# Kernel optimization log

Hardware: AMD Instinct MI355X
Metric: run time of the kernel (lower is better)

Reference implementation:

```python
import jax, jax.numpy as jnp
import numpy as np

NUM_GROUPS = 4   # temporal frames == deformable groups
K = 3            # deformable / fusion kernel size
PAD = 1
MAX_DISP = 7
STRIDE2 = 2


def _conv2d(x, w):
    # 3x3, stride 1, pad 1, no bias, NCHW/OIHW
    return jax.lax.conv_general_dilated(
        x, w, window_strides=(1, 1), padding=((PAD, PAD), (PAD, PAD)),
        dimension_numbers=("NCHW", "OIHW", "NCHW"))


def _correlation(x1, x2):
    """FlowNet/PWC correlation: kernel_size=1, max_displacement=7, stride1=1, stride2=2.
    Output: [B, 49, H, W], mean over channels of shifted dot products."""
    B, C, H, W = x1.shape
    r = MAX_DISP // STRIDE2          # 3 -> 7x7 displacement grid
    m = r * STRIDE2                  # 6 = max shift magnitude
    x2p = jnp.pad(x2, ((0, 0), (0, 0), (m, m), (m, m)))
    outs = []
    for di in range(-r, r + 1):
        for dj in range(-r, r + 1):
            dy, dx = di * STRIDE2, dj * STRIDE2
            sh = x2p[:, :, m + dy:m + dy + H, m + dx:m + dx + W]
            outs.append(jnp.mean(x1 * sh, axis=1))
    return jnp.stack(outs, axis=1)   # [B, 49, H, W]


def _deform_conv(x, offset, weight):
    """Deformable conv v1 (ConvOffset2d): 3x3, stride 1, pad 1, NUM_GROUPS deformable groups.
    offset: [B, G*2*K*K, H, W] laid out as (g, k, {dy,dx})."""
    B, C, H, W = x.shape
    G, K2 = NUM_GROUPS, K * K
    Cg = C // G
    off = offset.reshape(B, G, K2, 2, H, W)
    rel = (jnp.arange(K) - PAD).astype(x.dtype)
    rel_y = jnp.repeat(rel, K).reshape(1, 1, K2, 1, 1)   # kh-major, matches weight flatten
    rel_x = jnp.tile(rel, K).reshape(1, 1, K2, 1, 1)
    iy = jnp.arange(H, dtype=x.dtype).reshape(1, 1, 1, H, 1)
    ix = jnp.arange(W, dtype=x.dtype).reshape(1, 1, 1, 1, W)
    py = iy + rel_y + off[:, :, :, 0]   # [B,G,K2,H,W] sample rows
    px = ix + rel_x + off[:, :, :, 1]   # sample cols
    xg = x.reshape(B, G, Cg, H, W).transpose(0, 1, 3, 4, 2)  # [B,G,H,W,Cg]
    y0 = jnp.floor(py); x0 = jnp.floor(px)
    fy = py - y0; fx = px - x0
    y0 = y0.astype(jnp.int32); x0 = x0.astype(jnp.int32)
    bi = jnp.arange(B).reshape(B, 1, 1, 1, 1)
    gi = jnp.arange(G).reshape(1, G, 1, 1, 1)
    acc = jnp.zeros((B, G, K2, H, W, Cg), x.dtype)
    for dy in (0, 1):
        for dx in (0, 1):
            yy = y0 + dy; xx = x0 + dx
            wgt = (fy if dy else 1.0 - fy) * (fx if dx else 1.0 - fx)
            valid = ((yy >= 0) & (yy < H) & (xx >= 0) & (xx < W)).astype(x.dtype)
            v = xg[bi, gi, jnp.clip(yy, 0, H - 1), jnp.clip(xx, 0, W - 1)]
            acc = acc + v * (wgt * valid)[..., None]
    wr = weight.reshape(weight.shape[0], G, Cg, K2)  # [O,G,Cg,K2]
    return jnp.einsum('bgkhwc,ogck->bohw', acc, wr)


def setup_inputs() -> dict:
    key = jax.random.key(0)
    k0, k1, k2, k3 = jax.random.split(key, 4)
    B, C, H, W = 4, 256, 64, 64
    G = NUM_GROUPS
    inputs = jax.random.normal(k0, (B * G, C, H, W), jnp.float32)
    w_offset = jax.random.normal(k1, (G * 2 * K * K, C + MAX_DISP ** 2, K, K), jnp.float32) * 0.02
    w_def = jax.random.normal(k2, (C, C, K, K), jnp.float32) * 0.02
    w_fusion = jax.random.normal(k3, (C, C * G, K, K), jnp.float32) * 0.02
    return {"inputs": inputs, "w_offset": w_offset, "w_def": w_def,
            "w_fusion": w_fusion, "d1": 0, "d2": 0}


def reference(inputs, w_offset, w_def, w_fusion, d1, d2):
    # d1, d2 are unused by the original forward.
    G = NUM_GROUPS
    y = inputs[G - 1::G]
    _y = jax.lax.stop_gradient(y)
    feats = []
    for ii in range(G - 1):           # n_iter = 1
        x = inputs[ii::G]
        _x = jax.lax.stop_gradient(x)
        corr = _correlation(_x, _y)                       # [B,49,H,W]
        off = _conv2d(jnp.concatenate([x, corr], axis=1), w_offset)
        x = _deform_conv(x, off, w_def)
        feats.append(x)
    return _conv2d(jnp.concatenate(feats + [y], axis=1), w_fusion)
```

## Files before the change

kernel.cpp:

```cpp
#include <hip/hip_runtime.h>

#define HH 64
#define WW 64
#define HW 4096
#define CC 256
#define BB 4
#define GG 4
#define NPAIR 3

typedef __attribute__((ext_vector_type(8))) short short8;
typedef __attribute__((ext_vector_type(4))) float f32x4;
typedef unsigned short ushort_t;

__device__ inline ushort_t f2bf(float x) {
    unsigned int u = __float_as_uint(x);
    unsigned int r = (u + 0x7fffu + ((u >> 16) & 1u)) >> 16;
    return (ushort_t)r;
}
__device__ inline float bflo(unsigned u) { return __uint_as_float(u << 16); }
__device__ inline float bfhi(unsigned u) { return __uint_as_float(u & 0xffff0000u); }

__global__ void prep_wdef(const float* __restrict__ wd, ushort_t* __restrict__ wmf) {
    int idx = blockIdx.x * 256 + threadIdx.x;
    if (idx >= 9 * 256 * 256) return;
    int k = idx >> 16;
    int rem = idx & 65535;
    int o = rem >> 8;
    int c = rem & 255;
    wmf[idx] = f2bf(wd[((size_t)(o * 256 + c)) * 9 + k]);
}

__global__ void prep_woff(const float* __restrict__ wo, ushort_t* __restrict__ wmf) {
    int idx = blockIdx.x * 256 + threadIdx.x;
    if (idx >= 9 * 80 * 320) return;
    int k = idx / (80 * 320);
    int rem = idx % (80 * 320);
    int o = rem / 320;
    int ci = rem % 320;
    wmf[idx] = (o < 72 && ci < 305) ? f2bf(wo[((size_t)o * 305 + ci) * 9 + k]) : (ushort_t)0;
}

__global__ void prep_wfus(const float* __restrict__ wf, ushort_t* __restrict__ wmf) {
    int idx = blockIdx.x * 256 + threadIdx.x;
    if (idx >= 9 * 256 * 1024) return;
    int k = idx / (256 * 1024);
    int rem = idx % (256 * 1024);
    int o = rem / 1024;
    int ci = rem % 1024;
    wmf[idx] = f2bf(wf[((size_t)o * 1024 + ci) * 9 + k]);
}

__global__ void __launch_bounds__(256) xt_build(const float* __restrict__ in,
                                                ushort_t* __restrict__ XT) {
    __shared__ ushort_t tileT[64][72];
    int hw0 = blockIdx.x * 64;
    int ct = blockIdx.y;
    int z = blockIdx.z;
    int pair = z >> 2, b = z & 3;
    int t = threadIdx.x;
    int cil = t >> 2, q = t & 3;
    const float* sp = in + ((size_t)(b * 4 + pair) * 256 + ct * 64 + cil) * HW + hw0 + q * 16;
#pragma unroll
    for (int i = 0; i < 16; ++i) tileT[q * 16 + i][cil] = f2bf(sp[i]);
    __syncthreads();
    int hwl = t >> 2;
    const uint4* tp = reinterpret_cast<const uint4*>(&tileT[hwl][q * 16]);
    uint4* op = reinterpret_cast<uint4*>(
        &XT[((size_t)z * HW + hw0 + hwl) * 320 + ct * 64 + q * 16]);
    op[0] = tp[0];
    op[1] = tp[1];
}

__global__ void __launch_bounds__(256, 8) corr_partial(const float* __restrict__ in,
                                                       float* __restrict__ P) {
    __shared__ float x1l[8][64];
    __shared__ float x2l[8][7][76];
    int h = blockIdx.x, z = blockIdx.y, cg = blockIdx.z;
    int pair = z >> 2, b = z & 3;
    const float* x1 = in + (size_t)(b * GG + pair) * CC * HW + h * WW;
    const float* x2 = in + (size_t)(b * GG + 3) * CC * HW;
    int tid = threadIdx.x;
    int w = tid & 63;
    int dg = tid >> 6;

    float acc[2][7];
#pragma unroll
    for (int i = 0; i < 2; ++i)
#pragma unroll
        for (int j = 0; j < 7; ++j) acc[i][j] = 0.f;

    for (int c0 = cg * 64; c0 < cg * 64 + 64; c0 += 8) {
        __syncthreads();
#pragma unroll
        for (int idx = tid; idx < 512; idx += 256) {
            int cc = idx >> 6, ww = idx & 63;
            x1l[cc][ww] = x1[(size_t)(c0 + cc) * HW + ww];
        }
        for (int idx = tid; idx < 8 * 7 * 76; idx += 256) {
            int cc = idx / 532;
            int rem = idx - cc * 532;
            int r = rem / 76;
            int cl = rem - r * 76;
            int row = h + 2 * (r - 3);
            int col = cl - 6;
            float v = 0.f;
            if (row >= 0 && row < HH && col >= 0 && col < WW)
                v = x2[(size_t)(c0 + cc) * HW + row * WW + col];
            x2l[cc][r][cl] = v;
        }
        __syncthreads();
#pragma unroll
        for (int cc = 0; cc < 8; ++cc) {
            float x1v = x1l[cc][w];
#pragma unroll
            for (int i = 0; i < 2; ++i) {
                int di = dg * 2 + i;
                if (di < 7) {
#pragma unroll
                    for (int dj = 0; dj < 7; ++dj)
                        acc[i][dj] += x1v * x2l[cc][di][w + 2 * dj];
                }
            }
        }
    }
    float* pp = P + ((size_t)(cg * 12 + z) * 49) * HW + h * WW + w;
#pragma unroll
    for (int i = 0; i < 2; ++i) {
        int di = dg * 2 + i;
        if (di < 7) {
#pragma unroll
            for (int dj = 0; dj < 7; ++dj)
                pp[(size_t)(di * 7 + dj) * HW] = acc[i][dj];
        }
    }
}

__global__ void __launch_bounds__(256) corr_reduce(const float* __restrict__ P,
                                                   ushort_t* __restrict__ XT) {
    int h = blockIdx.x, z = blockIdx.y;
    int tid = threadIdx.x;
    int w = tid & 63;
    int dg = tid >> 6;
    const size_t cgs = (size_t)12 * 49 * HW;
    ushort_t* xrow = XT + ((size_t)z * HW + h * WW + w) * 320;
#pragma unroll
    for (int i = 0; i < 2; ++i) {
        int di = dg * 2 + i;
        if (di < 7) {
#pragma unroll
            for (int dj = 0; dj < 7; ++dj) {
                int d = di * 7 + dj;
                const float* pp = P + ((size_t)z * 49 + d) * HW + h * WW + w;
                float s = pp[0] + pp[cgs] + pp[2 * cgs] + pp[3 * cgs];
                xrow[256 + d] = f2bf(s * (1.f / 256.f));
            }
        }
    }
    if (dg == 3) {
#pragma unroll
        for (int p = 0; p < 15; ++p) xrow[305 + p] = 0;
    }
}

__global__ void __launch_bounds__(256, 2) offconv_mfma(const ushort_t* __restrict__ XT,
                                                       const ushort_t* __restrict__ wmf,
                                                       float* __restrict__ off) {
    __shared__ ushort_t a_lds[9][80][40];
    __shared__ ushort_t b_hal[264][40];
    int lin = (blockIdx.x & 7) * 48 + (blockIdx.x >> 3);
    int z = lin >> 5;
    int n0t = lin & 31;
    int h0 = n0t * 2;
    int t = threadIdx.x;
    int wid = t >> 6;
    int lane = t & 63;
    int l15 = lane & 15;
    int kq = lane >> 4;
    const ushort_t* xtb = XT + (size_t)z * HW * 320;

    f32x4 acc[5][2];
#pragma unroll
    for (int m = 0; m < 5; ++m)
#pragma unroll
        for (int n = 0; n < 2; ++n) acc[m][n] = (f32x4){0.f, 0.f, 0.f, 0.f};

#pragma unroll 1
    for (int cs = 0; cs < 10; ++cs) {
        int ci0 = cs * 32;
        __syncthreads();
        for (int idx = t; idx < 264; idx += 256) {
            int r = idx / 66, c = idx - r * 66;
            int hP = h0 + r - 1, wP = c - 1;
            uint4* dst = reinterpret_cast<uint4*>(&b_hal[idx][0]);
            if (hP >= 0 && hP < HH && wP >= 0 && wP < WW) {
                const uint4* src = reinterpret_cast<const uint4*>(
                    xtb + (size_t)(hP * WW + wP) * 320 + ci0);
                dst[0] = src[0];
                dst[1] = src[1];
                dst[2] = src[2];
                dst[3] = src[3];
            } else {
                uint4 zz = make_uint4(0, 0, 0, 0);
                dst[0] = zz;
                dst[1] = zz;
                dst[2] = zz;
                dst[3] = zz;
            }
        }
        for (int idx = t; idx < 2880; idx += 256) {
            int tp = idx / 320;
            int rem = idx - tp * 320;
            int o = rem >> 2, q = rem & 3;
            *reinterpret_cast<uint4*>(&a_lds[tp][o][q * 8]) =
                *reinterpret_cast<const uint4*>(
                    wmf + ((size_t)tp * 80 + o) * 320 + ci0 + q * 8);
        }
        __syncthreads();
#pragma unroll 1
        for (int tap = 0; tap < 9; ++tap) {
            int kh = tap / 3, kw = tap - kh * 3;
            short8 af[5], bf[2];
#pragma unroll
            for (int m = 0; m < 5; ++m)
                af[m] = *reinterpret_cast<const short8*>(&a_lds[tap][m * 16 + l15][kq * 8]);
#pragma unroll
            for (int n = 0; n < 2; ++n) {
                int p = wid * 32 + n * 16 + l15;
                int pos = ((p >> 6) + kh) * 66 + (p & 63) + kw;
                bf[n] = *reinterpret_cast<const short8*>(&b_hal[pos][kq * 8]);
            }
#pragma unroll
            for (int m = 0; m < 5; ++m)
#pragma unroll
                for (int n = 0; n < 2; ++n)
                    acc[m][n] = __builtin_amdgcn_mfma_f32_16x16x32_bf16(af[m], bf[n],
                                                                        acc[m][n], 0, 0, 0);
        }
    }
    float* ob = off + (size_t)z * 72 * HW + h0 * 64 + wid * 32;
#pragma unroll
    for (int m = 0; m < 5; ++m)
#pragma unroll
        for (int n = 0; n < 2; ++n)
#pragma unroll
            for (int e = 0; e < 4; ++e) {
                int o_l = m * 16 + kq * 4 + e;
                if (o_l < 72) ob[(size_t)o_l * HW + n * 16 + l15] = acc[m][n][e];
            }
}

__global__ void __launch_bounds__(256, 3) deform_mfma(const ushort_t* __restrict__ XT,
                                                      const float* __restrict__ off,
                                                      const ushort_t* __restrict__ wmf,
                                                      ushort_t* __restrict__ FT) {
    __shared__ ushort_t b_lds[64][264];
    int u = blockIdx.x & 7, v = blockIdx.x >> 3;
    int lin = u * 96 + v;
    int z = lin >> 6, h = lin & 63;
    int b = z & 3, pair = z >> 2;

    const ushort_t* xtz = XT + (size_t)z * HW * 320;
    const float* offp = off + (size_t)z * 72 * HW;
    int tid = threadIdx.x;
    int lane = tid & 63;
    int g = tid >> 6;
    int l15 = tid & 15;
    int kq = (tid >> 4) & 3;

    f32x4 acc[4][4];
#pragma unroll
    for (int m = 0; m < 4; ++m)
#pragma unroll
        for (int n = 0; n < 4; ++n) acc[m][n] = (f32x4){0.f, 0.f, 0.f, 0.f};

    for (int k = 0; k < 9; ++k) {
        __syncthreads();
        {
            float oy = offp[(size_t)(g * 18 + k * 2 + 0) * HW + h * WW + lane];
            float ox = offp[(size_t)(g * 18 + k * 2 + 1) * HW + h * WW + lane];
            float py = (float)h + (float)(k / 3 - 1) + oy;
            float px = (float)lane + (float)(k % 3 - 1) + ox;
            float y0f = floorf(py), x0f = floorf(px);
            float fy = py - y0f, fx = px - x0f;
            int y0 = (int)y0f, x0 = (int)x0f;
            int y1 = y0 + 1, x1 = x0 + 1;
            bool vy0 = (y0 >= 0) && (y0 < HH);
            bool vy1 = (y1 >= 0) && (y1 < HH);
            bool vx0 = (x0 >= 0) && (x0 < WW);
            bool vx1 = (x1 >= 0) && (x1 < WW);
            float w00 = (1.f - fy) * (1.f - fx) * ((vy0 && vx0) ? 1.f : 0.f);
            float w01 = (1.f - fy) * fx * ((vy0 && vx1) ? 1.f : 0.f);
            float w10 = fy * (1.f - fx) * ((vy1 && vx0) ? 1.f : 0.f);
            float w11 = fy * fx * ((vy1 && vx1) ? 1.f : 0.f);
            int cy0 = min(max(y0, 0), HH - 1), cy1 = min(max(y1, 0), HH - 1);
            int cx0 = min(max(x0, 0), WW - 1), cx1 = min(max(x1, 0), WW - 1);
            const ushort_t* p00 = xtz + (size_t)(cy0 * WW + cx0) * 320 + g * 64;
            const ushort_t* p01 = xtz + (size_t)(cy0 * WW + cx1) * 320 + g * 64;
            const ushort_t* p10 = xtz + (size_t)(cy1 * WW + cx0) * 320 + g * 64;
            const ushort_t* p11 = xtz + (size_t)(cy1 * WW + cx1) * 320 + g * 64;
#pragma unroll
            for (int c0 = 0; c0 < 64; c0 += 8) {
                uint4 a00 = *reinterpret_cast<const uint4*>(p00 + c0);
                uint4 a01 = *reinterpret_cast<const uint4*>(p01 + c0);
                uint4 a10 = *reinterpret_cast<const uint4*>(p10 + c0);
                uint4 a11 = *reinterpret_cast<const uint4*>(p11 + c0);
                unsigned pw[4];
                const unsigned* u00 = &a00.x;
                const unsigned* u01 = &a01.x;
                const unsigned* u10 = &a10.x;
                const unsigned* u11 = &a11.x;
#pragma unroll
                for (int q = 0; q < 4; ++q) {
                    float s0 = w00 * bflo(u00[q]) + w01 * bflo(u01[q]) +
                               w10 * bflo(u10[q]) + w11 * bflo(u11[q]);
                    float s1 = w00 * bfhi(u00[q]) + w01 * bfhi(u01[q]) +
                               w10 * bfhi(u10[q]) + w11 * bfhi(u11[q]);
                    pw[q] = (unsigned)f2bf(s0) | ((unsigned)f2bf(s1) << 16);
                }
                *reinterpret_cast<uint4*>(&b_lds[lane][g * 64 + c0]) =
                    make_uint4(pw[0], pw[1], pw[2], pw[3]);
            }
        }
        __syncthreads();
        const ushort_t* wkbase = wmf + (size_t)k * 65536 + (size_t)(g * 64) * 256;
#pragma unroll 1
        for (int cs = 0; cs < 8; ++cs) {
            int c0 = cs * 32;
            short8 bfr[4], afr[4];
#pragma unroll
            for (int n = 0; n < 4; ++n)
                bfr[n] = *reinterpret_cast<const short8*>(&b_lds[n * 16 + l15][c0 + kq * 8]);
#pragma unroll
            for (int m = 0; m < 4; ++m)
                afr[m] = *reinterpret_cast<const short8*>(
                    wkbase + (size_t)(m * 16 + l15) * 256 + c0 + kq * 8);
#pragma unroll
            for (int m = 0; m < 4; ++m)
#pragma unroll
                for (int n = 0; n < 4; ++n)
                    acc[m][n] = __builtin_amdgcn_mfma_f32_16x16x32_bf16(afr[m], bfr[n],
                                                                        acc[m][n], 0, 0, 0);
        }
    }
    __syncthreads();
#pragma unroll
    for (int m = 0; m < 4; ++m)
#pragma unroll
        for (int n = 0; n < 4; ++n) {
            unsigned lo = (unsigned)f2bf(acc[m][n][0]) | ((unsigned)f2bf(acc[m][n][1]) << 16);
            unsigned hi = (unsigned)f2bf(acc[m][n][2]) | ((unsigned)f2bf(acc[m][n][3]) << 16);
            uint2 vv = make_uint2(lo, hi);
            *reinterpret_cast<uint2*>(&b_lds[n * 16 + l15][g * 64 + m * 16 + kq * 4]) = vv;
        }
    __syncthreads();
    int wout = tid >> 2, ch = tid & 3;
    ushort_t* dst = FT + ((size_t)b * HW + h * 64 + wout) * 1024 + pair * 256 + ch * 64;
    const ushort_t* srcl = &b_lds[wout][ch * 64];
#pragma unroll
    for (int i = 0; i < 8; ++i) {
        uint4 vv = *reinterpret_cast<const uint4*>(srcl + i * 8);
        *reinterpret_cast<uint4*>(dst + i * 8) = vv;
    }
}

__global__ void __launch_bounds__(256) ft_build_y(const float* __restrict__ in,
                                                  ushort_t* __restrict__ FT) {
    __shared__ ushort_t tileT[64][72];
    int hw0 = blockIdx.x * 64;
    int ct = blockIdx.y;
    int b = blockIdx.z;
    int t = threadIdx.x;
    int cil = t >> 2, q = t & 3;
    const float* sp = in + ((size_t)(b * 4 + 3) * 256 + ct * 64 + cil) * HW + hw0 + q * 16;
#pragma unroll
    for (int i = 0; i < 16; ++i) tileT[q * 16 + i][cil] = f2bf(sp[i]);
    __syncthreads();
    int hwl = t >> 2;
    const uint4* tp = reinterpret_cast<const uint4*>(&tileT[hwl][q * 16]);
    uint4* op = reinterpret_cast<uint4*>(
        &FT[((size_t)b * HW + hw0 + hwl) * 1024 + 768 + ct * 64 + q * 16]);
    op[0] = tp[0];
    op[1] = tp[1];
}

__global__ void __launch_bounds__(256, 2) fusion_mfma(const ushort_t* __restrict__ FT,
                                                      const ushort_t* __restrict__ wmf,
                                                      float* __restrict__ out) {
    __shared__ ushort_t a_lds[9][64][40];
    __shared__ ushort_t b_hal[264][40];
    int lin = ((blockIdx.x & 7) << 6) | (blockIdx.x >> 3);
    int ot = lin & 3;
    int g2 = lin >> 2;
    int n0t = g2 & 31;
    int b = g2 >> 5;
    int o0 = ot * 64;
    int h0 = n0t * 2;
    int t = threadIdx.x;
    int wid = t >> 6;
    int lane = t & 63;
    int l15 = lane & 15;
    int kq = lane >> 4;
    const ushort_t* ftb = FT + (size_t)b * HW * 1024;

    f32x4 acc[4][2];
#pragma unroll
    for (int fm = 0; fm < 4; ++fm)
#pragma unroll
        for (int fn = 0; fn < 2; ++fn) acc[fm][fn] = (f32x4){0.f, 0.f, 0.f, 0.f};

#pragma unroll 1
    for (int cs = 0; cs < 32; ++cs) {
        int ci0 = cs * 32;
        __syncthreads();
        for (int idx = t; idx < 264; idx += 256) {
            int r = idx / 66, c = idx - r * 66;
            int hP = h0 + r - 1, wP = c - 1;
            uint4* dst = reinterpret_cast<uint4*>(&b_hal[idx][0]);
            if (hP >= 0 && hP < HH && wP >= 0 && wP < WW) {
                const uint4* src = reinterpret_cast<const uint4*>(
                    ftb + (size_t)(hP * WW + wP) * 1024 + ci0);
                dst[0] = src[0];
                dst[1] = src[1];
                dst[2] = src[2];
                dst[3] = src[3];
            } else {
                uint4 zz = make_uint4(0, 0, 0, 0);
                dst[0] = zz;
                dst[1] = zz;
                dst[2] = zz;
                dst[3] = zz;
            }
        }
        for (int idx = t; idx < 2304; idx += 256) {
            int tp = idx >> 8;
            int rem = idx & 255;
            int o = rem >> 2, q = rem & 3;
            *reinterpret_cast<uint4*>(&a_lds[tp][o][q * 8]) =
                *reinterpret_cast<const uint4*>(
                    wmf + ((size_t)(tp * 256 + o0 + o) << 10) + ci0 + q * 8);
        }
        __syncthreads();
#pragma unroll 1
        for (int tap = 0; tap < 9; ++tap) {
            int kh = tap / 3, kw = tap - kh * 3;
            short8 af[4], bf[2];
#pragma unroll
            for (int m = 0; m < 4; ++m)
                af[m] = *reinterpret_cast<const short8*>(&a_lds[tap][m * 16 + l15][kq * 8]);
#pragma unroll
            for (int n = 0; n < 2; ++n) {
                int p = wid * 32 + n * 16 + l15;
                int pos = ((p >> 6) + kh) * 66 + (p & 63) + kw;
                bf[n] = *reinterpret_cast<const short8*>(&b_hal[pos][kq * 8]);
            }
#pragma unroll
            for (int m = 0; m < 4; ++m)
#pragma unroll
                for (int n = 0; n < 2; ++n)
                    acc[m][n] = __builtin_amdgcn_mfma_f32_16x16x32_bf16(af[m], bf[n],
                                                                        acc[m][n], 0, 0, 0);
        }
    }
    float* ob = out + ((size_t)b * 256 + o0) * HW + h0 * 64 + wid * 32;
#pragma unroll
    for (int fm = 0; fm < 4; ++fm)
#pragma unroll
        for (int fn = 0; fn < 2; ++fn)
#pragma unroll
            for (int e = 0; e < 4; ++e) {
                int o_l = fm * 16 + 4 * kq + e;
                ob[(size_t)o_l * HW + fn * 16 + l15] = acc[fm][fn][e];
            }
}

extern "C" void kernel_launch(void* const* d_in, const int* in_sizes, int n_in,
                              void* d_out, int out_size, void* d_ws, size_t ws_size,
                              hipStream_t stream) {
    const float* in   = (const float*)d_in[0];
    const float* wOff = (const float*)d_in[1];
    const float* wDef = (const float*)d_in[2];
    const float* wFus = (const float*)d_in[3];
    float* out = (float*)d_out;
    char* base = (char*)d_ws;

    ushort_t* XT     = (ushort_t*)base;
    ushort_t* FT     = (ushort_t*)(base + 31457280);
    float* corrP     = (float*)(base + 31457280);
    float* offB      = (float*)(base + 65011712);
    ushort_t* wdefMF = (ushort_t*)(base + 79167488);
    ushort_t* woffMF = (ushort_t*)(base + 80347136);
    ushort_t* wfusMF = (ushort_t*)(base + 80807936);

    hipLaunchKernelGGL(prep_wdef, dim3((9 * 256 * 256 + 255) / 256), dim3(256), 0, stream,
                       wDef, wdefMF);
    hipLaunchKernelGGL(prep_woff, dim3((9 * 80 * 320 + 255) / 256), dim3(256), 0, stream,
                       wOff, woffMF);
    hipLaunchKernelGGL(prep_wfus, dim3((9 * 256 * 1024 + 255) / 256), dim3(256), 0, stream,
                       wFus, wfusMF);
    hipLaunchKernelGGL(xt_build, dim3(64, 4, 12), dim3(256), 0, stream, in, XT);
    hipLaunchKernelGGL(corr_partial, dim3(64, 12, 4), dim3(256), 0, stream, in, corrP);
    hipLaunchKernelGGL(corr_reduce, dim3(64, 12), dim3(256), 0, stream, corrP, XT);
    hipLaunchKernelGGL(offconv_mfma, dim3(384), dim3(256), 0, stream, XT, woffMF, offB);
    hipLaunchKernelGGL(ft_build_y, dim3(64, 4, 4), dim3(256), 0, stream, in, FT);
    hipLaunchKernelGGL(deform_mfma, dim3(768), dim3(256), 0, stream, XT, offB, wdefMF, FT);
    hipLaunchKernelGGL(fusion_mfma, dim3(512), dim3(256), 0, stream, FT, wfusMF, out);
}
```

Measured before the change: 582.5 us.

## Double-buffer fusion halo, read weights directly from global, merge weight prep

The three weight-prep kernels are merged into one launch to cut launch overhead. In offconv and fusion the A-operand weights are no longer staged through shared memory and are loaded straight from global memory per tap. The fusion kernel now double-buffers the activation halo in LDS, prefetching the next channel slice while the current one is computed, with one barrier per iteration. This lowers LDS use and barrier count, and may raise occupancy, but it relies on cache hits for repeated weight loads and may add global-load latency to the MFMA loop.

New measurement: 773.9 us. 32.9% more time.

```diff
diff --git a/kernel.cpp b/kernel.cpp
--- a/kernel.cpp
+++ b/kernel.cpp
@@ -20,34 +20,36 @@
 __device__ inline float bflo(unsigned u) { return __uint_as_float(u << 16); }
 __device__ inline float bfhi(unsigned u) { return __uint_as_float(u & 0xffff0000u); }
 
-__global__ void prep_wdef(const float* __restrict__ wd, ushort_t* __restrict__ wmf) {
+__global__ void prep_all(const float* __restrict__ wd, const float* __restrict__ wo,
+                         const float* __restrict__ wf, ushort_t* __restrict__ wdefMF,
+                         ushort_t* __restrict__ woffMF, ushort_t* __restrict__ wfusMF) {
     int idx = blockIdx.x * 256 + threadIdx.x;
-    if (idx >= 9 * 256 * 256) return;
-    int k = idx >> 16;
-    int rem = idx & 65535;
-    int o = rem >> 8;
-    int c = rem & 255;
-    wmf[idx] = f2bf(wd[((size_t)(o * 256 + c)) * 9 + k]);
-}
-
-__global__ void prep_woff(const float* __restrict__ wo, ushort_t* __restrict__ wmf) {
-    int idx = blockIdx.x * 256 + threadIdx.x;
-    if (idx >= 9 * 80 * 320) return;
-    int k = idx / (80 * 320);
-    int rem = idx % (80 * 320);
-    int o = rem / 320;
-    int ci = rem % 320;
-    wmf[idx] = (o < 72 && ci < 305) ? f2bf(wo[((size_t)o * 305 + ci) * 9 + k]) : (ushort_t)0;
-}
-
-__global__ void prep_wfus(const float* __restrict__ wf, ushort_t* __restrict__ wmf) {
-    int idx = blockIdx.x * 256 + threadIdx.x;
-    if (idx >= 9 * 256 * 1024) return;
-    int k = idx / (256 * 1024);
-    int rem = idx % (256 * 1024);
-    int o = rem / 1024;
-    int ci = rem % 1024;
-    wmf[idx] = f2bf(wf[((size_t)o * 1024 + ci) * 9 + k]);
+    if (idx < 589824) {
+        int k = idx >> 16;
+        int rem = idx & 65535;
+        int o = rem >> 8;
+        int c = rem & 255;
+        wdefMF[idx] = f2bf(wd[((size_t)(o * 256 + c)) * 9 + k]);
+        return;
+    }
+    idx -= 589824;
+    if (idx < 230400) {
+        int k = idx / (80 * 320);
+        int rem = idx % (80 * 320);
+        int o = rem / 320;
+        int ci = rem % 320;
+        woffMF[idx] = (o < 72 && ci < 305) ? f2bf(wo[((size_t)o * 305 + ci) * 9 + k])
+                                           : (ushort_t)0;
+        return;
+    }
+    idx -= 230400;
+    if (idx < 2359296) {
+        int k = idx / (256 * 1024);
+        int rem = idx % (256 * 1024);
+        int o = rem / 1024;
+        int ci = rem % 1024;
+        wfusMF[idx] = f2bf(wf[((size_t)o * 1024 + ci) * 9 + k]);
+    }
 }
 
 __global__ void __launch_bounds__(256) xt_build(const float* __restrict__ in,
@@ -165,7 +167,6 @@
 __global__ void __launch_bounds__(256, 2) offconv_mfma(const ushort_t* __restrict__ XT,
                                                        const ushort_t* __restrict__ wmf,
                                                        float* __restrict__ off) {
-    __shared__ ushort_t a_lds[9][80][40];
     __shared__ ushort_t b_hal[264][40];
     int lin = (blockIdx.x & 7) * 48 + (blockIdx.x >> 3);
     int z = lin >> 5;
@@ -207,14 +208,6 @@
                 dst[3] = zz;
             }
         }
-        for (int idx = t; idx < 2880; idx += 256) {
-            int tp = idx / 320;
-            int rem = idx - tp * 320;
-            int o = rem >> 2, q = rem & 3;
-            *reinterpret_cast<uint4*>(&a_lds[tp][o][q * 8]) =
-                *reinterpret_cast<const uint4*>(
-                    wmf + ((size_t)tp * 80 + o) * 320 + ci0 + q * 8);
-        }
         __syncthreads();
 #pragma unroll 1
         for (int tap = 0; tap < 9; ++tap) {
@@ -222,7 +215,8 @@
             short8 af[5], bf[2];
 #pragma unroll
             for (int m = 0; m < 5; ++m)
-                af[m] = *reinterpret_cast<const short8*>(&a_lds[tap][m * 16 + l15][kq * 8]);
+                af[m] = *reinterpret_cast<const short8*>(
+                    wmf + ((size_t)tap * 80 + m * 16 + l15) * 320 + ci0 + kq * 8);
 #pragma unroll
             for (int n = 0; n < 2; ++n) {
                 int p = wid * 32 + n * 16 + l15;
@@ -386,8 +380,7 @@
 __global__ void __launch_bounds__(256, 2) fusion_mfma(const ushort_t* __restrict__ FT,
                                                       const ushort_t* __restrict__ wmf,
                                                       float* __restrict__ out) {
-    __shared__ ushort_t a_lds[9][64][40];
-    __shared__ ushort_t b_hal[264][40];
+    __shared__ ushort_t b_hal[2][264][40];
     int lin = ((blockIdx.x & 7) << 6) | (blockIdx.x >> 3);
     int ot = lin & 3;
     int g2 = lin >> 2;
@@ -408,14 +401,12 @@
 #pragma unroll
         for (int fn = 0; fn < 2; ++fn) acc[fm][fn] = (f32x4){0.f, 0.f, 0.f, 0.f};
 
-#pragma unroll 1
-    for (int cs = 0; cs < 32; ++cs) {
+    auto stage_b = [&](int cs, int bsel) {
         int ci0 = cs * 32;
-        __syncthreads();
         for (int idx = t; idx < 264; idx += 256) {
             int r = idx / 66, c = idx - r * 66;
             int hP = h0 + r - 1, wP = c - 1;
-            uint4* dst = reinterpret_cast<uint4*>(&b_hal[idx][0]);
+            uint4* dst = reinterpret_cast<uint4*>(&b_hal[bsel][idx][0]);
             if (hP >= 0 && hP < HH && wP >= 0 && wP < WW) {
                 const uint4* src = reinterpret_cast<const uint4*>(
                     ftb + (size_t)(hP * WW + wP) * 1024 + ci0);
@@ -431,27 +422,28 @@
                 dst[3] = zz;
             }
         }
-        for (int idx = t; idx < 2304; idx += 256) {
-            int tp = idx >> 8;
-            int rem = idx & 255;
-            int o = rem >> 2, q = rem & 3;
-            *reinterpret_cast<uint4*>(&a_lds[tp][o][q * 8]) =
-                *reinterpret_cast<const uint4*>(
-                    wmf + ((size_t)(tp * 256 + o0 + o) << 10) + ci0 + q * 8);
-        }
-        __syncthreads();
+    };
+
+    stage_b(0, 0);
+    __syncthreads();
+#pragma unroll 1
+    for (int cs = 0; cs < 32; ++cs) {
+        int ci0 = cs * 32;
+        int bsel = cs & 1;
+        if (cs < 31) stage_b(cs + 1, bsel ^ 1);
 #pragma unroll 1
         for (int tap = 0; tap < 9; ++tap) {
             int kh = tap / 3, kw = tap - kh * 3;
             short8 af[4], bf[2];
 #pragma unroll
             for (int m = 0; m < 4; ++m)
-                af[m] = *reinterpret_cast<const short8*>(&a_lds[tap][m * 16 + l15][kq * 8]);
+                af[m] = *reinterpret_cast<const short8*>(
+                    wmf + ((size_t)(tap * 256 + o0 + m * 16 + l15) << 10) + ci0 + kq * 8);
 #pragma unroll
             for (int n = 0; n < 2; ++n) {
                 int p = wid * 32 + n * 16 + l15;
                 int pos = ((p >> 6) + kh) * 66 + (p & 63) + kw;
-                bf[n] = *reinterpret_cast<const short8*>(&b_hal[pos][kq * 8]);
+                bf[n] = *reinterpret_cast<const short8*>(&b_hal[bsel][pos][kq * 8]);
             }
 #pragma unroll
             for (int m = 0; m < 4; ++m)
@@ -460,6 +452,7 @@
                     acc[m][n] = __builtin_amdgcn_mfma_f32_16x16x32_bf16(af[m], bf[n],
                                                                         acc[m][n], 0, 0, 0);
         }
+        __syncthreads();
     }
     float* ob = out + ((size_t)b * 256 + o0) * HW + h0 * 64 + wid * 32;
 #pragma unroll
@@ -491,12 +484,8 @@
     ushort_t* woffMF = (ushort_t*)(base + 80347136);
     ushort_t* wfusMF = (ushort_t*)(base + 80807936);
 
-    hipLaunchKernelGGL(prep_wdef, dim3((9 * 256 * 256 + 255) / 256), dim3(256), 0, stream,
-                       wDef, wdefMF);
-    hipLaunchKernelGGL(prep_woff, dim3((9 * 80 * 320 + 255) / 256), dim3(256), 0, stream,
-                       wOff, woffMF);
-    hipLaunchKernelGGL(prep_wfus, dim3((9 * 256 * 1024 + 255) / 256), dim3(256), 0, stream,
-                       wFus, wfusMF);
+    hipLaunchKernelGGL(prep_all, dim3((3179520 + 255) / 256), dim3(256), 0, stream,
+                       wDef, wOff, wFus, wdefMF, woffMF, wfusMF);
     hipLaunchKernelGGL(xt_build, dim3(64, 4, 12), dim3(256), 0, stream, in, XT);
     hipLaunchKernelGGL(corr_partial, dim3(64, 12, 4), dim3(256), 0, stream, in, corrP);
     hipLaunchKernelGGL(corr_reduce, dim3(64, 12), dim3(256), 0, stream, corrP, XT);
```
